# Optimization experiments

Measured on AMD Instinct MI355X. Metric: run time of the kernel, lower is better.

Reference implementation:

```python
import jax, jax.numpy as jnp
import numpy as np

N_NODES = 100000
N_EDGES = 1600000
IN_DIM = 64
HID = 64
N_LAYERS = 2
BN_EPS = 1e-5


def setup_inputs() -> dict:
    key = jax.random.key(0)
    ks = jax.random.split(key, 10)
    s = 0.02
    return {
        "x": jax.random.normal(ks[0], (N_NODES, IN_DIM), dtype=jnp.float32),
        "edge_index": jax.random.randint(ks[1], (2, N_EDGES), 0, N_NODES),
        "edge_attr": jax.random.uniform(ks[2], (N_EDGES,), dtype=jnp.float32),
        "lin_W": jax.random.normal(ks[3], (IN_DIM, HID), dtype=jnp.float32) * s,
        "lin_b": jnp.zeros((HID,), dtype=jnp.float32),
        "eenc_w": jax.random.normal(ks[4], (HID,), dtype=jnp.float32) * s,
        "eenc_b": jnp.zeros((HID,), dtype=jnp.float32),
        "conv_W": jax.random.normal(ks[5], (N_LAYERS, HID, HID), dtype=jnp.float32) * s,
        "conv_b": jnp.zeros((N_LAYERS, HID), dtype=jnp.float32),
        "bn_gamma": jnp.ones((N_LAYERS, HID), dtype=jnp.float32),
        "bn_beta": jnp.zeros((N_LAYERS, HID), dtype=jnp.float32),
    }


def _forward(x, edge_index, edge_attr, lin_W, lin_b, eenc_w, eenc_b,
             conv_W, conv_b, bn_gamma, bn_beta):
    n = x.shape[0]
    src, dst = edge_index[0], edge_index[1]
    # input projection (in_dim > 1 -> lin_layer branch)
    h = x @ lin_W + lin_b                                  # [N, HID]
    e = edge_attr[:, None] * eenc_w[None, :] + eenc_b      # [E, HID]
    h0 = h
    h = h.at[src].set(jax.nn.relu(h0[src] + e))
    h = h.at[dst].set(jax.nn.relu(h0[dst] + e))
    # GCN normalization with self-loops (weight 1), shared across layers
    loops = jnp.arange(n)
    s2 = jnp.concatenate([src, loops])
    d2 = jnp.concatenate([dst, loops])
    w2 = jnp.concatenate([edge_attr, jnp.ones((n,), dtype=h.dtype)])
    deg = jax.ops.segment_sum(w2, d2, num_segments=n)
    dinv = jnp.where(deg > 0, 1.0 / jnp.sqrt(jnp.where(deg > 0, deg, 1.0)), 0.0)
    norm = dinv[s2] * w2 * dinv[d2]                        # [E+N]
    h_list = []
    for l in range(N_LAYERS):
        xw = h @ conv_W[l]                                 # [N, HID]
        agg = jax.ops.segment_sum(norm[:, None] * xw[s2], d2, num_segments=n)
        agg = agg + conv_b[l]
        mean = jnp.mean(agg, axis=0)
        var = jnp.mean((agg - mean) ** 2, axis=0)          # biased, as BN uses
        hn = (agg - mean) / jnp.sqrt(var + BN_EPS) * bn_gamma[l] + bn_beta[l]
        # dropout is identity (eval mode); relu on all but last layer
        h = hn if l == N_LAYERS - 1 else jax.nn.relu(hn)
        h_list.append(h)
    return jnp.concatenate(h_list, axis=1)                 # [N, N_LAYERS*HID]


def reference(x, edge_index, edge_attr, lin_W, lin_b, eenc_w, eenc_b,
              conv_W, conv_b, bn_gamma, bn_beta):
    return _forward(x, edge_index, edge_attr, lin_W, lin_b, eenc_w, eenc_b,
                    conv_W, conv_b, bn_gamma, bn_beta)
```

## Files before the change

### kernel.cpp

```cpp
#include <hip/hip_runtime.h>
#include <hip/hip_fp16.h>

#define N_NODES 100000
#define N_EDGES 1600000
#define BN_EPS 1e-5f
#define NBLK_E 6250
#define NBLK_G 3125
#define NBLK_N 391
#define NBINS 391
#define BCAP 4608
#define PT 4096
#define NPART 391
#define OVF_CAP 32768
#define A18 262144.0f
#define A18_INV 3.814697265625e-6f
typedef unsigned long long ull;
typedef unsigned int uint;


__global__ void init_kernel(int* gcnt, int* win, uint* zbitmap, int* flags, float* bnacc) {
    int v = blockIdx.x * blockDim.x + threadIdx.x;
    if (v < N_NODES) win[v] = -1;
    if (v < NBINS) gcnt[v] = 0;
    if (v < 3125) zbitmap[v] = 0;
    if (v < 2) flags[v] = 0;
    if (v < 256) bnacc[v] = 0.0f;
}

__launch_bounds__(256)
__global__ void partition_gemm(const int* __restrict__ src, const int* __restrict__ dst,
                               const float* __restrict__ attr,
                               ull* __restrict__ bucket, int* __restrict__ gcnt,
                               int* __restrict__ flags, int* __restrict__ ovf_b,
                               ull* __restrict__ ovf_e,
                               const float* __restrict__ x, const float* __restrict__ lin_W,
                               const float* __restrict__ lin_b, float* __restrict__ h0) {
    __shared__ ull ent[PT];
    __shared__ unsigned short ebin[PT];
    __shared__ int hist[NBINS];
    __shared__ int cur[NBINS];
    __shared__ int gdel[NBINS];
    __shared__ int sc[512];
    int t = threadIdx.x;
    if (blockIdx.x < NPART) {
        int e0 = blockIdx.x * PT;
        int n = N_EDGES - e0; if (n > PT) n = PT;
        for (int b = t; b < NBINS; b += 256) hist[b] = 0;
        __syncthreads();
        for (int k = t; k < n; k += 256) atomicAdd(&hist[dst[e0 + k] >> 8], 1);
        __syncthreads();
        sc[t] = (t < NBINS) ? hist[t] : 0;
        sc[t + 256] = (t + 256 < NBINS) ? hist[t + 256] : 0;
        __syncthreads();
        for (int off = 1; off < 512; off <<= 1) {
            int a0 = sc[t] + ((t >= off) ? sc[t - off] : 0);
            int a1 = sc[t + 256] + sc[t + 256 - off];
            __syncthreads();
            sc[t] = a0; sc[t + 256] = a1;
            __syncthreads();
        }
        for (int b = t; b < NBINS; b += 256) {
            int lb = sc[b] - hist[b];
            cur[b] = lb;
            int gb = atomicAdd(&gcnt[b], hist[b]);
            gdel[b] = gb - lb;
        }
        __syncthreads();
        for (int k = t; k < n; k += 256) {
            int i = e0 + k;
            int d = dst[i];
            uint aq = (uint)(attr[i] * A18); if (aq > 0x3FFFFu) aq = 0x3FFFFu;
            int bin = d >> 8;
            ull e = ((ull)(d & 255) << 56) | ((ull)i << 35) | ((ull)src[i] << 18) | aq;
            int p = atomicAdd(&cur[bin], 1);
            ent[p] = e;
            ebin[p] = (unsigned short)bin;
        }
        __syncthreads();
        for (int k = t; k < n; k += 256) {
            int b = ebin[k];
            int off = k + gdel[b];
            if (off < BCAP) bucket[(size_t)b * BCAP + off] = ent[k];
            else {
                int q = atomicAdd(&flags[1], 1);
                if (q < OVF_CAP) { ovf_b[q] = b; ovf_e[q] = ent[k]; }
            }
        }
        return;
    }
    float* xs = (float*)ent;
    int lane = t & 63, w = t >> 6;
    int base = (blockIdx.x - NPART) * 32;
    const float4* Xv = (const float4*)(x + (size_t)base * 64);
    float4* xsv = (float4*)xs;
    xsv[t] = Xv[t];
    xsv[t + 256] = Xv[t + 256];
    float wc[64];
    #pragma unroll
    for (int k = 0; k < 64; ++k) wc[k] = lin_W[k * 64 + lane];
    __syncthreads();
    float bval = lin_b[lane];
    for (int rr = 0; rr < 8; ++rr) {
        int rl = w * 8 + rr;
        float acc = bval;
        #pragma unroll
        for (int k = 0; k < 64; ++k) acc = fmaf(xs[rl * 64 + k], wc[k], acc);
        h0[(size_t)(base + rl) * 64 + lane] = acc;
    }
}

__launch_bounds__(256)
__global__ void finalize_reorder(const ull* __restrict__ bucket, const int* __restrict__ gcnt,
                                 const int* __restrict__ ovf_b, const ull* __restrict__ ovf_e,
                                 int* __restrict__ flags, uint* __restrict__ zbitmap,
                                 float* __restrict__ dinv, float* __restrict__ wa,
                                 ull* __restrict__ csr2, int* __restrict__ startv,
                                 int* __restrict__ lenv) {
    __shared__ ull ent[BCAP];
    __shared__ int cnt[256];
    __shared__ int sc[256];
    __shared__ int cur[256];
    __shared__ int cbase[257];
    int t = threadIdx.x, b = blockIdx.x;
    int len = gcnt[b], blen = len < BCAP ? len : BCAP;
    const ull* bb = bucket + (size_t)b * BCAP;
    cnt[t] = 0;
    __syncthreads();
    ull r[18];
    #pragma unroll
    for (int k = 0; k < 18; ++k) {
        int j = k * 256 + t;
        r[k] = 0;
        if (j < blen) {
            ull e = bb[j];
            r[k] = e;
            atomicAdd(&cnt[(int)(e >> 56)], 1);
        }
    }
    __syncthreads();
    sc[t] = cnt[t];
    __syncthreads();
    for (int off = 1; off < 256; off <<= 1) {
        int a = sc[t] + ((t >= off) ? sc[t - off] : 0);
        __syncthreads();
        sc[t] = a;
        __syncthreads();
    }
    cbase[t + 1] = sc[t];
    if (t == 0) cbase[0] = 0;
    cur[t] = sc[t] - cnt[t];
    __syncthreads();
    #pragma unroll
    for (int k = 0; k < 18; ++k) {
        int j = k * 256 + t;
        if (j < blen) {
            ull e = r[k];
            int p = atomicAdd(&cur[(int)(e >> 56)], 1);
            ent[p] = e;
        }
    }
    __syncthreads();
    size_t base = (size_t)b * BCAP;
    for (int k = t; k < blen; k += 256) {
        ull e = ent[k];
        csr2[base + k] = (((ull)(e & 0x3FFFFull)) << 32) | ((e >> 18) & 0x1FFFFull);
    }
    int j0 = cbase[t], j1 = cbase[t + 1];
    float sum = 0.0f; uint winx = 0, wat = 0;
    for (int j = j0; j < j1; ++j) {
        ull e = ent[j];
        uint aq = (uint)(e & 0x3FFFFull);
        sum += (float)aq * A18_INV;
        uint ei = (uint)((e >> 35) & 0x1FFFFFull) + 1u;
        if (ei > winx) { winx = ei; wat = aq; }
    }
    if (len > BCAP) {
        int oc = flags[1]; if (oc > OVF_CAP) oc = OVF_CAP;
        for (int q = 0; q < oc; ++q) {
            if (ovf_b[q] != b) continue;
            ull e = ovf_e[q];
            if ((int)(e >> 56) != t) continue;
            uint aq = (uint)(e & 0x3FFFFull);
            sum += (float)aq * A18_INV;
            uint ei = (uint)((e >> 35) & 0x1FFFFFull) + 1u;
            if (ei > winx) { winx = ei; wat = aq; }
        }
    }
    int v = b * 256 + t;
    if (v < N_NODES) {
        dinv[v] = rsqrtf(1.0f + sum);
        startv[v] = (int)(base + j0);
        lenv[v] = j1 - j0;
        if (winx > 0) {
            wa[v] = (float)wat * A18_INV;
        } else {
            wa[v] = -1.0f;
            atomicOr(&zbitmap[v >> 5], 1u << (v & 31));
            flags[0] = 1;
        }
    }
}

__global__ void fixup_scan(const int* __restrict__ src, const int* __restrict__ flags,
                           const uint* __restrict__ zbitmap, int* __restrict__ win) {
    if (flags[0] == 0) return;
    int i = blockIdx.x * 256 + threadIdx.x;
    int s = src[i];
    if ((zbitmap[s >> 5] >> (s & 31)) & 1u) atomicMax(&win[s], i);
}

__global__ void fixup_apply(const int* __restrict__ flags, const uint* __restrict__ zbitmap,
                            const int* __restrict__ win, const float* __restrict__ attr,
                            float* __restrict__ wa) {
    if (flags[0] == 0) return;
    int v = blockIdx.x * 256 + threadIdx.x;
    if (v >= N_NODES) return;
    if (((zbitmap[v >> 5] >> (v & 31)) & 1u) && win[v] >= 0) wa[v] = attr[win[v]];
}

__launch_bounds__(256)
__global__ void gemm_l0_nrm(const float* __restrict__ h0, const float* __restrict__ W,
                            const float* __restrict__ wa, const float* __restrict__ ew,
                            const float* __restrict__ eb, __half* __restrict__ xw16,
                            ull* __restrict__ csr2, const int* __restrict__ gcnt,
                            const float* __restrict__ dinv) {
    __shared__ float xs[2048];
    int t = threadIdx.x;
    if (blockIdx.x < NBINS) {
        int b = blockIdx.x;
        int len = gcnt[b], blen = len < BCAP ? len : BCAP;
        ull* c = csr2 + (size_t)b * BCAP;
        for (int k = t; k < blen; k += 256) {
            ull pk = c[k];
            uint s = (uint)pk;
            float np = (float)(uint)(pk >> 32) * A18_INV * dinv[s];
            c[k] = ((ull)__float_as_uint(np) << 32) | s;
        }
        return;
    }
    int lane = t & 63, w = t >> 6;
    int base = (blockIdx.x - NBINS) * 32;
    const float4* Hv = (const float4*)(h0 + (size_t)base * 64);
    #pragma unroll
    for (int q = 0; q < 2; ++q) {
        int idx = t + q * 256;
        int rl = idx >> 4, f0 = (idx & 15) * 4;
        float4 v = Hv[idx];
        float wav = wa[base + rl];
        if (wav >= 0.0f) {
            v.x = fmaxf(fmaf(wav, ew[f0 + 0], v.x + eb[f0 + 0]), 0.0f);
            v.y = fmaxf(fmaf(wav, ew[f0 + 1], v.y + eb[f0 + 1]), 0.0f);
            v.z = fmaxf(fmaf(wav, ew[f0 + 2], v.z + eb[f0 + 2]), 0.0f);
            v.w = fmaxf(fmaf(wav, ew[f0 + 3], v.w + eb[f0 + 3]), 0.0f);
        }
        ((float4*)xs)[idx] = v;
    }
    float wc[64];
    #pragma unroll
    for (int k = 0; k < 64; ++k) wc[k] = W[k * 64 + lane];
    __syncthreads();
    for (int rr = 0; rr < 8; ++rr) {
        int rl = w * 8 + rr;
        float acc = 0.0f;
        #pragma unroll
        for (int k = 0; k < 64; ++k) acc = fmaf(xs[rl * 64 + k], wc[k], acc);
        xw16[(size_t)(base + rl) * 64 + lane] = __float2half(acc);
    }
}

__launch_bounds__(256)
__global__ void gemm_l1(const float* __restrict__ agg, const float* __restrict__ bnacc,
                        const float* __restrict__ gamma, const float* __restrict__ beta,
                        const float* __restrict__ W, float* __restrict__ out,
                        __half* __restrict__ xw16) {
    __shared__ float xs[2048];
    int t = threadIdx.x, lane = t & 63, w = t >> 6;
    int base = blockIdx.x * 32;
    const float4* Av = (const float4*)(agg + (size_t)base * 64);
    const float invN = 1.0f / (float)N_NODES;
    #pragma unroll
    for (int q = 0; q < 2; ++q) {
        int idx = t + q * 256;
        int rl = idx >> 4, f0 = (idx & 15) * 4;
        float4 v = Av[idx];
        float vv[4] = {v.x, v.y, v.z, v.w};
        #pragma unroll
        for (int c = 0; c < 4; ++c) {
            int f = f0 + c;
            float mean = bnacc[f] * invN;
            float var = bnacc[64 + f] * invN - mean * mean;
            float scl = gamma[f] * rsqrtf(var + BN_EPS);
            float bs = beta[f] - mean * scl;
            vv[c] = fmaxf(fmaf(vv[c], scl, bs), 0.0f);
        }
        float4 r = {vv[0], vv[1], vv[2], vv[3]};
        ((float4*)xs)[idx] = r;
        *(float4*)(out + (size_t)(base + rl) * 128 + f0) = r;
    }
    float wc[64];
    #pragma unroll
    for (int k = 0; k < 64; ++k) wc[k] = W[k * 64 + lane];
    __syncthreads();
    for (int rr = 0; rr < 8; ++rr) {
        int rl = w * 8 + rr;
        float acc = 0.0f;
        #pragma unroll
        for (int k = 0; k < 64; ++k) acc = fmaf(xs[rl * 64 + k], wc[k], acc);
        xw16[(size_t)(base + rl) * 64 + lane] = __float2half(acc);
    }
}

__launch_bounds__(256)
__global__ void gather4(const __half* __restrict__ xw16, const ull* __restrict__ csr2,
                        const int* __restrict__ startv, const int* __restrict__ lenv,
                        const float* __restrict__ dinv, const int* __restrict__ gcnt,
                        const int* __restrict__ flags, const int* __restrict__ ovf_b,
                        const ull* __restrict__ ovf_e,
                        const float* __restrict__ convb, float* __restrict__ agg,
                        float* __restrict__ bnacc) {
    __shared__ float reds[4][64];
    __shared__ float redq[4][64];
    int t = threadIdx.x, lane = t & 63, w = t >> 6;
    int ng = lane >> 4, fl = lane & 15, f0 = fl * 4, ngb = ng << 4;
    float cb0 = convb[f0], cb1 = convb[f0 + 1], cb2 = convb[f0 + 2], cb3 = convb[f0 + 3];
    float s0 = 0.f, s1 = 0.f, s2 = 0.f, s3 = 0.f;
    float q0 = 0.f, q1 = 0.f, q2 = 0.f, q3 = 0.f;
    int ovfn = flags[1];
    for (int v = blockIdx.x * 16 + w * 4 + ng; v < N_NODES; v += 32768) {
        float dv = dinv[v];
        int sb = startv[v], ln = lenv[v];
        float2 raw = *(const float2*)(xw16 + (size_t)v * 64 + f0);
        float2 xv01 = __half22float2(*(__half2*)&raw.x);
        float2 xv23 = __half22float2(*(__half2*)&raw.y);
        float w2 = dv * dv;
        float a0 = w2 * xv01.x, a1 = w2 * xv01.y, a2 = w2 * xv23.x, a3 = w2 * xv23.y;
        float b0 = 0.f, b1 = 0.f, b2 = 0.f, b3 = 0.f;
        for (int c0 = 0; c0 < ln; c0 += 16) {
            int m = ln - c0; if (m > 16) m = 16;
            ull pk = (fl < m) ? csr2[sb + c0 + fl] : 0ull;
            int j = 0;
            for (; j + 4 <= m; j += 4) {
                ull pA = __shfl(pk, ngb + j, 64);
                ull pB = __shfl(pk, ngb + j + 1, 64);
                ull pC = __shfl(pk, ngb + j + 2, 64);
                ull pD = __shfl(pk, ngb + j + 3, 64);
                float2 rA = *(const float2*)(xw16 + (size_t)(uint)pA * 64 + f0);
                float2 rB = *(const float2*)(xw16 + (size_t)(uint)pB * 64 + f0);
                float2 rC = *(const float2*)(xw16 + (size_t)(uint)pC * 64 + f0);
                float2 rD = *(const float2*)(xw16 + (size_t)(uint)pD * 64 + f0);
                float nA = __uint_as_float((uint)(pA >> 32)) * dv;
                float nB = __uint_as_float((uint)(pB >> 32)) * dv;
                float nC = __uint_as_float((uint)(pC >> 32)) * dv;
                float nD = __uint_as_float((uint)(pD >> 32)) * dv;
                float2 xA01 = __half22float2(*(__half2*)&rA.x);
                float2 xA23 = __half22float2(*(__half2*)&rA.y);
                float2 xB01 = __half22float2(*(__half2*)&rB.x);
                float2 xB23 = __half22float2(*(__half2*)&rB.y);
                float2 xC01 = __half22float2(*(__half2*)&rC.x);
                float2 xC23 = __half22float2(*(__half2*)&rC.y);
                float2 xD01 = __half22float2(*(__half2*)&rD.x);
                float2 xD23 = __half22float2(*(__half2*)&rD.y);
                a0 = fmaf(nA, xA01.x, a0); a1 = fmaf(nA, xA01.y, a1);
                a2 = fmaf(nA, xA23.x, a2); a3 = fmaf(nA, xA23.y, a3);
                b0 = fmaf(nB, xB01.x, b0); b1 = fmaf(nB, xB01.y, b1);
                b2 = fmaf(nB, xB23.x, b2); b3 = fmaf(nB, xB23.y, b3);
                a0 = fmaf(nC, xC01.x, a0); a1 = fmaf(nC, xC01.y, a1);
                a2 = fmaf(nC, xC23.x, a2); a3 = fmaf(nC, xC23.y, a3);
                b0 = fmaf(nD, xD01.x, b0); b1 = fmaf(nD, xD01.y, b1);
                b2 = fmaf(nD, xD23.x, b2); b3 = fmaf(nD, xD23.y, b3);
            }
            for (; j < m; ++j) {
                ull pA = __shfl(pk, ngb + j, 64);
                float2 rA = *(const float2*)(xw16 + (size_t)(uint)pA * 64 + f0);
                float nA = __uint_as_float((uint)(pA >> 32)) * dv;
                float2 xA01 = __half22float2(*(__half2*)&rA.x);
                float2 xA23 = __half22float2(*(__half2*)&rA.y);
                a0 = fmaf(nA, xA01.x, a0); a1 = fmaf(nA, xA01.y, a1);
                a2 = fmaf(nA, xA23.x, a2); a3 = fmaf(nA, xA23.y, a3);
            }
        }
        float t0 = a0 + b0, t1 = a1 + b1, t2 = a2 + b2, t3 = a3 + b3;
        if (ovfn > 0 && gcnt[v >> 8] > BCAP) {
            int oc = ovfn; if (oc > OVF_CAP) oc = OVF_CAP;
            int ld = v & 255, b = v >> 8;
            for (int q = 0; q < oc; ++q) {
                if (ovf_b[q] != b) continue;
                ull e = ovf_e[q];
                if ((int)(e >> 56) != ld) continue;
                uint s = (uint)((e >> 18) & 0x1FFFFull);
                float nr = (float)(uint)(e & 0x3FFFFull) * A18_INV * dinv[s] * dv;
                float2 rr = *(const float2*)(xw16 + (size_t)s * 64 + f0);
                float2 x01 = __half22float2(*(__half2*)&rr.x);
                float2 x23 = __half22float2(*(__half2*)&rr.y);
                t0 = fmaf(nr, x01.x, t0); t1 = fmaf(nr, x01.y, t1);
                t2 = fmaf(nr, x23.x, t2); t3 = fmaf(nr, x23.y, t3);
            }
        }
        t0 += cb0; t1 += cb1; t2 += cb2; t3 += cb3;
        *(float4*)(agg + (size_t)v * 64 + f0) = make_float4(t0, t1, t2, t3);
        s0 += t0; q0 += t0 * t0;
        s1 += t1; q1 += t1 * t1;
        s2 += t2; q2 += t2 * t2;
        s3 += t3; q3 += t3 * t3;
    }
    s0 += __shfl_xor(s0, 16, 64); s0 += __shfl_xor(s0, 32, 64);
    s1 += __shfl_xor(s1, 16, 64); s1 += __shfl_xor(s1, 32, 64);
    s2 += __shfl_xor(s2, 16, 64); s2 += __shfl_xor(s2, 32, 64);
    s3 += __shfl_xor(s3, 16, 64); s3 += __shfl_xor(s3, 32, 64);
    q0 += __shfl_xor(q0, 16, 64); q0 += __shfl_xor(q0, 32, 64);
    q1 += __shfl_xor(q1, 16, 64); q1 += __shfl_xor(q1, 32, 64);
    q2 += __shfl_xor(q2, 16, 64); q2 += __shfl_xor(q2, 32, 64);
    q3 += __shfl_xor(q3, 16, 64); q3 += __shfl_xor(q3, 32, 64);
    if (ng == 0) {
        reds[w][f0] = s0; reds[w][f0 + 1] = s1; reds[w][f0 + 2] = s2; reds[w][f0 + 3] = s3;
        redq[w][f0] = q0; redq[w][f0 + 1] = q1; redq[w][f0 + 2] = q2; redq[w][f0 + 3] = q3;
    }
    __syncthreads();
    if (t < 64) {
        float ss = reds[0][t] + reds[1][t] + reds[2][t] + reds[3][t];
        float qq = redq[0][t] + redq[1][t] + redq[2][t] + redq[3][t];
        atomicAdd(&bnacc[t], ss);
        atomicAdd(&bnacc[64 + t], qq);
    }
}

__launch_bounds__(256)
__global__ void bn_final(const float* __restrict__ agg, const float* __restrict__ bnacc,
                         const float* __restrict__ gamma, const float* __restrict__ beta,
                         float* __restrict__ out) {
    int idx = blockIdx.x * 256 + threadIdx.x;
    int c = idx & 63, v = idx >> 6;
    const float invN = 1.0f / (float)N_NODES;
    float mean = bnacc[c] * invN;
    float var = bnacc[64 + c] * invN - mean * mean;
    float scl = gamma[c] * rsqrtf(var + BN_EPS);
    float bs = beta[c] - mean * scl;
    out[(size_t)v * 128 + 64 + c] = fmaf(agg[idx], scl, bs);
}

extern "C" void kernel_launch(void* const* d_in, const int* in_sizes, int n_in,
                              void* d_out, int out_size, void* d_ws, size_t ws_size,
                              hipStream_t stream) {
    const float* x      = (const float*)d_in[0];
    const int*   eidx   = (const int*)d_in[1];
    const float* attr   = (const float*)d_in[2];
    const float* lin_W  = (const float*)d_in[3];
    const float* lin_b  = (const float*)d_in[4];
    const float* eenc_w = (const float*)d_in[5];
    const float* eenc_b = (const float*)d_in[6];
    const float* conv_W = (const float*)d_in[7];
    const float* conv_b = (const float*)d_in[8];
    const float* gamma  = (const float*)d_in[9];
    const float* beta   = (const float*)d_in[10];
    float* out = (float*)d_out;

    const int* src = eidx;
    const int* dst = eidx + N_EDGES;

    char* p = (char*)d_ws;
    ull* bucket = (ull*)p;   p += (size_t)NBINS * BCAP * 8;
    ull* csr2   = (ull*)p;   p += (size_t)NBINS * BCAP * 8;
    ull* ovf_e  = (ull*)p;   p += (size_t)OVF_CAP * 8;
    float* h0   = (float*)p; p += (size_t)N_NODES * 64 * 4;
    __half* xw16 = (__half*)p; p += (size_t)N_NODES * 64 * 2;
    float* dinv = (float*)p; p += (size_t)N_NODES * 4;
    float* wa   = (float*)p; p += (size_t)N_NODES * 4;
    int* win    = (int*)p;   p += (size_t)N_NODES * 4;
    int* startv = (int*)p;   p += (size_t)N_NODES * 4;
    int* lenv   = (int*)p;   p += (size_t)N_NODES * 4;
    int* ovf_b  = (int*)p;   p += (size_t)OVF_CAP * 4;
    int* gcnt   = (int*)p;   p += (NBINS + 1) * 4 + 20;
    uint* zbitmap = (uint*)p; p += 3125 * 4 + 12;
    int* flags  = (int*)p;   p += 64;
    float* bnacc = (float*)p; p += 256 * 4;
    float* agg = h0;

    init_kernel<<<NBLK_N, 256, 0, stream>>>(gcnt, win, zbitmap, flags, bnacc);
    partition_gemm<<<NPART + NBLK_G, 256, 0, stream>>>(src, dst, attr, bucket, gcnt,
                                                       flags, ovf_b, ovf_e,
                                                       x, lin_W, lin_b, h0);
    finalize_reorder<<<NBINS, 256, 0, stream>>>(bucket, gcnt, ovf_b, ovf_e,
                                                flags, zbitmap, dinv, wa,
                                                csr2, startv, lenv);
    fixup_scan<<<NBLK_E, 256, 0, stream>>>(src, flags, zbitmap, win);
    fixup_apply<<<NBLK_N, 256, 0, stream>>>(flags, zbitmap, win, attr, wa);

    gemm_l0_nrm<<<NBINS + NBLK_G, 256, 0, stream>>>(h0, conv_W, wa, eenc_w, eenc_b,
                                                    xw16, csr2, gcnt, dinv);
    gather4<<<2048, 256, 0, stream>>>(xw16, csr2, startv, lenv, dinv, gcnt,
                                      flags, ovf_b, ovf_e, conv_b, agg, bnacc);
    gemm_l1<<<NBLK_G, 256, 0, stream>>>(agg, bnacc, gamma, beta,
                                        conv_W + 64 * 64, out, xw16);
    gather4<<<2048, 256, 0, stream>>>(xw16, csr2, startv, lenv, dinv, gcnt,
                                      flags, ovf_b, ovf_e, conv_b + 64, agg, bnacc + 128);
    bn_final<<<25000, 256, 0, stream>>>(agg, bnacc + 128, gamma + 64, beta + 64, out);
}
```

Before: 439.3 us.

## Compress CSR edge entries to 32-bit with half-precision norm and nontemporal memory ops

Each CSR edge entry now packs a 17-bit source index with a truncated fp16 edge norm into one 32-bit word, held in a new csr3 buffer. This halves the index traffic read by both gather passes. The gather loop also prefetches the next 16-edge chunk of packed entries before processing the current one. Many streaming stores and loads (bucket, csr, out, agg) become nontemporal to reduce cache pollution. The cost is lower precision in the norm weights: fp16 with the low mantissa bit dropped.

```diff
diff --git a/kernel.cpp b/kernel.cpp
--- a/kernel.cpp
+++ b/kernel.cpp
@@ -16,6 +16,8 @@
 #define A18_INV 3.814697265625e-6f
 typedef unsigned long long ull;
 typedef unsigned int uint;
+typedef unsigned short ushort;
+typedef float v4f __attribute__((ext_vector_type(4)));
 
 
 __global__ void init_kernel(int* gcnt, int* win, uint* zbitmap, int* flags, float* bnacc) {
@@ -80,7 +82,7 @@
         for (int k = t; k < n; k += 256) {
             int b = ebin[k];
             int off = k + gdel[b];
-            if (off < BCAP) bucket[(size_t)b * BCAP + off] = ent[k];
+            if (off < BCAP) __builtin_nontemporal_store(ent[k], &bucket[(size_t)b * BCAP + off]);
             else {
                 int q = atomicAdd(&flags[1], 1);
                 if (q < OVF_CAP) { ovf_b[q] = b; ovf_e[q] = ent[k]; }
@@ -132,7 +134,7 @@
         int j = k * 256 + t;
         r[k] = 0;
         if (j < blen) {
-            ull e = bb[j];
+            ull e = __builtin_nontemporal_load(&bb[j]);
             r[k] = e;
             atomicAdd(&cnt[(int)(e >> 56)], 1);
         }
@@ -163,7 +165,8 @@
     size_t base = (size_t)b * BCAP;
     for (int k = t; k < blen; k += 256) {
         ull e = ent[k];
-        csr2[base + k] = (((ull)(e & 0x3FFFFull)) << 32) | ((e >> 18) & 0x1FFFFull);
+        ull packed = (((ull)(e & 0x3FFFFull)) << 32) | ((e >> 18) & 0x1FFFFull);
+        __builtin_nontemporal_store(packed, &csr2[base + k]);
     }
     int j0 = cbase[t], j1 = cbase[t + 1];
     float sum = 0.0f; uint winx = 0, wat = 0;
@@ -222,19 +225,21 @@
 __global__ void gemm_l0_nrm(const float* __restrict__ h0, const float* __restrict__ W,
                             const float* __restrict__ wa, const float* __restrict__ ew,
                             const float* __restrict__ eb, __half* __restrict__ xw16,
-                            ull* __restrict__ csr2, const int* __restrict__ gcnt,
-                            const float* __restrict__ dinv) {
+                            const ull* __restrict__ csr2, uint* __restrict__ csr3,
+                            const int* __restrict__ gcnt, const float* __restrict__ dinv) {
     __shared__ float xs[2048];
     int t = threadIdx.x;
     if (blockIdx.x < NBINS) {
         int b = blockIdx.x;
         int len = gcnt[b], blen = len < BCAP ? len : BCAP;
-        ull* c = csr2 + (size_t)b * BCAP;
+        const ull* c2 = csr2 + (size_t)b * BCAP;
+        uint* c3 = csr3 + (size_t)b * BCAP;
         for (int k = t; k < blen; k += 256) {
-            ull pk = c[k];
+            ull pk = __builtin_nontemporal_load(&c2[k]);
             uint s = (uint)pk;
             float np = (float)(uint)(pk >> 32) * A18_INV * dinv[s];
-            c[k] = ((ull)__float_as_uint(np) << 32) | s;
+            ushort hb = __half_as_ushort(__float2half(np));
+            __builtin_nontemporal_store(((uint)(hb >> 1) << 17) | s, &c3[k]);
         }
         return;
     }
@@ -295,7 +300,8 @@
         }
         float4 r = {vv[0], vv[1], vv[2], vv[3]};
         ((float4*)xs)[idx] = r;
-        *(float4*)(out + (size_t)(base + rl) * 128 + f0) = r;
+        v4f rv = {vv[0], vv[1], vv[2], vv[3]};
+        __builtin_nontemporal_store(rv, (v4f*)(out + (size_t)(base + rl) * 128 + f0));
     }
     float wc[64];
     #pragma unroll
@@ -311,7 +317,7 @@
 }
 
 __launch_bounds__(256)
-__global__ void gather4(const __half* __restrict__ xw16, const ull* __restrict__ csr2,
+__global__ void gather4(const __half* __restrict__ xw16, const uint* __restrict__ csr3,
                         const int* __restrict__ startv, const int* __restrict__ lenv,
                         const float* __restrict__ dinv, const int* __restrict__ gcnt,
                         const int* __restrict__ flags, const int* __restrict__ ovf_b,
@@ -335,23 +341,26 @@
         float w2 = dv * dv;
         float a0 = w2 * xv01.x, a1 = w2 * xv01.y, a2 = w2 * xv23.x, a3 = w2 * xv23.y;
         float b0 = 0.f, b1 = 0.f, b2 = 0.f, b3 = 0.f;
+        uint pk = (fl < ln) ? __builtin_nontemporal_load(&csr3[sb + fl]) : 0u;
         for (int c0 = 0; c0 < ln; c0 += 16) {
             int m = ln - c0; if (m > 16) m = 16;
-            ull pk = (fl < m) ? csr2[sb + c0 + fl] : 0ull;
+            uint pkc = pk;
+            int nc = c0 + 16;
+            if (nc < ln) pk = (fl < ln - nc) ? __builtin_nontemporal_load(&csr3[sb + nc + fl]) : 0u;
             int j = 0;
             for (; j + 4 <= m; j += 4) {
-                ull pA = __shfl(pk, ngb + j, 64);
-                ull pB = __shfl(pk, ngb + j + 1, 64);
-                ull pC = __shfl(pk, ngb + j + 2, 64);
-                ull pD = __shfl(pk, ngb + j + 3, 64);
-                float2 rA = *(const float2*)(xw16 + (size_t)(uint)pA * 64 + f0);
-                float2 rB = *(const float2*)(xw16 + (size_t)(uint)pB * 64 + f0);
-                float2 rC = *(const float2*)(xw16 + (size_t)(uint)pC * 64 + f0);
-                float2 rD = *(const float2*)(xw16 + (size_t)(uint)pD * 64 + f0);
-                float nA = __uint_as_float((uint)(pA >> 32)) * dv;
-                float nB = __uint_as_float((uint)(pB >> 32)) * dv;
-                float nC = __uint_as_float((uint)(pC >> 32)) * dv;
-                float nD = __uint_as_float((uint)(pD >> 32)) * dv;
+                uint pA = __shfl(pkc, ngb + j, 64);
+                uint pB = __shfl(pkc, ngb + j + 1, 64);
+                uint pC = __shfl(pkc, ngb + j + 2, 64);
+                uint pD = __shfl(pkc, ngb + j + 3, 64);
+                float2 rA = *(const float2*)(xw16 + (size_t)(pA & 0x1FFFFu) * 64 + f0);
+                float2 rB = *(const float2*)(xw16 + (size_t)(pB & 0x1FFFFu) * 64 + f0);
+                float2 rC = *(const float2*)(xw16 + (size_t)(pC & 0x1FFFFu) * 64 + f0);
+                float2 rD = *(const float2*)(xw16 + (size_t)(pD & 0x1FFFFu) * 64 + f0);
+                float nA = __half2float(__ushort_as_half((ushort)((pA >> 17) << 1))) * dv;
+                float nB = __half2float(__ushort_as_half((ushort)((pB >> 17) << 1))) * dv;
+                float nC = __half2float(__ushort_as_half((ushort)((pC >> 17) << 1))) * dv;
+                float nD = __half2float(__ushort_as_half((ushort)((pD >> 17) << 1))) * dv;
                 float2 xA01 = __half22float2(*(__half2*)&rA.x);
                 float2 xA23 = __half22float2(*(__half2*)&rA.y);
                 float2 xB01 = __half22float2(*(__half2*)&rB.x);
@@ -370,9 +379,9 @@
                 b2 = fmaf(nD, xD23.x, b2); b3 = fmaf(nD, xD23.y, b3);
             }
             for (; j < m; ++j) {
-                ull pA = __shfl(pk, ngb + j, 64);
-                float2 rA = *(const float2*)(xw16 + (size_t)(uint)pA * 64 + f0);
-                float nA = __uint_as_float((uint)(pA >> 32)) * dv;
+                uint pA = __shfl(pkc, ngb + j, 64);
+                float2 rA = *(const float2*)(xw16 + (size_t)(pA & 0x1FFFFu) * 64 + f0);
+                float nA = __half2float(__ushort_as_half((ushort)((pA >> 17) << 1))) * dv;
                 float2 xA01 = __half22float2(*(__half2*)&rA.x);
                 float2 xA23 = __half22float2(*(__half2*)&rA.y);
                 a0 = fmaf(nA, xA01.x, a0); a1 = fmaf(nA, xA01.y, a1);
@@ -397,7 +406,8 @@
             }
         }
         t0 += cb0; t1 += cb1; t2 += cb2; t3 += cb3;
-        *(float4*)(agg + (size_t)v * 64 + f0) = make_float4(t0, t1, t2, t3);
+        v4f rv = {t0, t1, t2, t3};
+        __builtin_nontemporal_store(rv, (v4f*)(agg + (size_t)v * 64 + f0));
         s0 += t0; q0 += t0 * t0;
         s1 += t1; q1 += t1 * t1;
         s2 += t2; q2 += t2 * t2;
@@ -435,7 +445,7 @@
     float var = bnacc[64 + c] * invN - mean * mean;
     float scl = gamma[c] * rsqrtf(var + BN_EPS);
     float bs = beta[c] - mean * scl;
-    out[(size_t)v * 128 + 64 + c] = fmaf(agg[idx], scl, bs);
+    __builtin_nontemporal_store(fmaf(agg[idx], scl, bs), &out[(size_t)v * 128 + 64 + c]);
 }
 
 extern "C" void kernel_launch(void* const* d_in, const int* in_sizes, int n_in,
@@ -460,6 +470,7 @@
     char* p = (char*)d_ws;
     ull* bucket = (ull*)p;   p += (size_t)NBINS * BCAP * 8;
     ull* csr2   = (ull*)p;   p += (size_t)NBINS * BCAP * 8;
+    uint* csr3  = (uint*)p;  p += (size_t)NBINS * BCAP * 4;
     ull* ovf_e  = (ull*)p;   p += (size_t)OVF_CAP * 8;
     float* h0   = (float*)p; p += (size_t)N_NODES * 64 * 4;
     __half* xw16 = (__half*)p; p += (size_t)N_NODES * 64 * 2;
@@ -486,12 +497,12 @@
     fixup_apply<<<NBLK_N, 256, 0, stream>>>(flags, zbitmap, win, attr, wa);
 
     gemm_l0_nrm<<<NBINS + NBLK_G, 256, 0, stream>>>(h0, conv_W, wa, eenc_w, eenc_b,
-                                                    xw16, csr2, gcnt, dinv);
-    gather4<<<2048, 256, 0, stream>>>(xw16, csr2, startv, lenv, dinv, gcnt,
+                                                    xw16, csr2, csr3, gcnt, dinv);
+    gather4<<<2048, 256, 0, stream>>>(xw16, csr3, startv, lenv, dinv, gcnt,
                                       flags, ovf_b, ovf_e, conv_b, agg, bnacc);
     gemm_l1<<<NBLK_G, 256, 0, stream>>>(agg, bnacc, gamma, beta,
                                         conv_W + 64 * 64, out, xw16);
-    gather4<<<2048, 256, 0, stream>>>(xw16, csr2, startv, lenv, dinv, gcnt,
+    gather4<<<2048, 256, 0, stream>>>(xw16, csr3, startv, lenv, dinv, gcnt,
                                       flags, ovf_b, ovf_e, conv_b + 64, agg, bnacc + 128);
     bn_final<<<25000, 256, 0, stream>>>(agg, bnacc + 128, gamma + 64, beta + 64, out);
 }
```

Measured after the change: 447.7 us. Within noise of the previous version (+1.9%).
